# Kernel tuning notes

Hardware: AMD Instinct MI355X
Metric: run time of the kernel (lower is better)

The kernel has to match this reference:

```python
import jax, jax.numpy as jnp
import numpy as np

B, IN_CH, OUT_CH, T, N_STATE, FACTOR = 8, 128, 128, 16384, 256, 2
DT = 1.0
LN_EPS = 1e-5


def setup_inputs() -> dict:
    key = jax.random.key(0)
    k = jax.random.split(key, 5)
    x = jax.random.normal(k[0], (B, IN_CH, T), jnp.float32)
    raw_lambda = jnp.zeros((N_STATE,), jnp.float32)
    B_c = jax.random.normal(k[1], (IN_CH, N_STATE), jnp.float32) * (1.0 / np.sqrt(IN_CH))
    C_mat = jax.random.normal(k[2], (N_STATE, OUT_CH), jnp.float32) * (1.0 / np.sqrt(N_STATE))
    ln_gamma = jnp.ones((OUT_CH,), jnp.float32)
    ln_beta = jnp.zeros((OUT_CH,), jnp.float32)
    # Conv1d(out_ch*factor, out_ch, kernel_size=1): weight (out, in), bias (out,)
    W = jax.random.normal(k[3], (OUT_CH, OUT_CH * FACTOR), jnp.float32) * (1.0 / np.sqrt(OUT_CH * FACTOR))
    b = jax.random.normal(k[4], (OUT_CH,), jnp.float32) * 0.01
    return {"x": x, "raw_lambda": raw_lambda, "B_c": B_c, "C_mat": C_mat,
            "ln_gamma": ln_gamma, "ln_beta": ln_beta, "W": W, "b": b}


def reference(x, raw_lambda, B_c, C_mat, ln_gamma, ln_beta, W, b):
    # --- SSMLayerZOH ---
    lam = -jax.nn.softplus(raw_lambda)              # (N,) continuous diag, < 0
    A_d = jnp.exp(lam * DT)                         # ZOH discretized diag
    B_d = B_c * ((A_d - 1.0) / lam)[None, :]        # (IN, N)
    v = jnp.einsum('bct,cn->tbn', x, B_d)           # per-step input injection

    def step(s, vt):
        s = s * A_d + vt
        return s, s

    s0 = jnp.zeros((x.shape[0], lam.shape[0]), x.dtype)
    _, ss = jax.lax.scan(step, s0, v)               # (T, B, N)
    y = jnp.einsum('tbn,no->bto', ss, C_mat)        # (B, T, OUT)

    # --- LayerNorm(out_ch) + SiLU ---
    mu = jnp.mean(y, axis=-1, keepdims=True)
    var = jnp.mean((y - mu) ** 2, axis=-1, keepdims=True)
    h = (y - mu) / jnp.sqrt(var + LN_EPS) * ln_gamma + ln_beta
    h = h * jax.nn.sigmoid(h)                       # SiLU

    # --- Resample (factor > 1 branch): downsample T, stack factor into channels ---
    h = jnp.transpose(h, (0, 2, 1))                 # (B, OUT, T)
    Bn, C, Tt = h.shape
    hr = h.reshape(Bn, C, Tt // FACTOR, FACTOR)
    hr = jnp.transpose(hr, (0, 1, 3, 2)).reshape(Bn, C * FACTOR, Tt // FACTOR)
    out = jnp.einsum('bct,oc->bot', hr, W) + b[None, :, None]  # conv1x1
    return out
```

## Files before the change

kernel.cpp:

```cpp
#include <hip/hip_runtime.h>

#define BATCH 8
#define CIN 128
#define OCH 128
#define T_LEN 16384
#define NS 256
#define CHUNK 64
#define NCHUNK (T_LEN / CHUNK)
#define THALF (T_LEN / 2)
#define SCHUNK 8192
#define HROW 132
#define NCHK 8

typedef __attribute__((ext_vector_type(8))) short bf16x8;
typedef __attribute__((ext_vector_type(4))) float f32x4;
typedef __attribute__((ext_vector_type(4))) unsigned int u32x4;

__device__ __forceinline__ unsigned int pk2(float lo, float hi) {
  unsigned int d;
  asm("v_cvt_pk_bf16_f32 %0, %1, %2" : "=v"(d) : "v"(lo), "v"(hi));
  return d;
}
__device__ __forceinline__ unsigned short f2bf(float f) {
  unsigned int u = __float_as_uint(f);
  u += 0x7fffu + ((u >> 16) & 1u);
  return (unsigned short)(u >> 16);
}
__device__ __forceinline__ float softplusf_(float v) {
  return (v > 20.0f) ? v : log1pf(expf(v));
}
__device__ __forceinline__ void rawbar() {
  __builtin_amdgcn_sched_barrier(0);
  asm volatile("s_waitcnt lgkmcnt(0)" ::: "memory");
  __builtin_amdgcn_sched_barrier(0);
  __builtin_amdgcn_s_barrier();
  __builtin_amdgcn_sched_barrier(0);
}

__global__ __launch_bounds__(256) void k_prep(
    const float* __restrict__ rl, const float* __restrict__ Bc,
    const float* __restrict__ Cm, const float* __restrict__ W,
    unsigned short* __restrict__ BdT, unsigned short* __restrict__ CT,
    unsigned short* __restrict__ Wb, float* __restrict__ Ad, float* __restrict__ rL,
    float* __restrict__ PWf)
{
  const int tid = blockIdx.x * 256 + threadIdx.x;
  if (tid < NS * CIN) {
    const int n = tid >> 7, c = tid & 127;
    float lam = -softplusf_(rl[n]);
    float ad = expf(lam);
    float sc = (ad - 1.0f) / lam;
    BdT[tid] = f2bf(Bc[c * NS + n] * sc);
  } else if (tid < 2 * NS * CIN) {
    const int i = tid - NS * CIN;
    const int o = i >> 8, n = i & 255;
    CT[i] = f2bf(Cm[n * OCH + o]);
  } else if (tid < 3 * NS * CIN) {
    const int i = tid - 2 * NS * CIN;
    Wb[i] = f2bf(W[i]);
  } else if (tid < 3 * NS * CIN + NS) {
    const int n = tid - 3 * NS * CIN;
    float lam = -softplusf_(rl[n]);
    Ad[n] = expf(lam);
    rL[n] = expf(lam * (float)CHUNK);
  } else if (tid < 3 * NS * CIN + NS + 32 * NS) {
    const int i = tid - (3 * NS * CIN + NS);
    const int tp = i >> 8, n = i & 255;
    float lam = -softplusf_(rl[n]);
    PWf[i] = expf(lam * (float)(2 * tp + 1));
  }
}

__global__ __launch_bounds__(256) void k_combine(float* __restrict__ carry,
                                                 const float* __restrict__ rL)
{
  const int b = blockIdx.x >> 5;
  const int ng = blockIdx.x & 31;
  const int t = threadIdx.x;
  __shared__ float Y[8][NCHUNK];
  float* base = carry + ((size_t)b * NCHUNK + t) * NS + ng * 8;
  #pragma unroll
  for (int i4 = 0; i4 < 2; ++i4) {
    float4 q = *(const float4*)(base + i4 * 4);
    Y[i4 * 4 + 0][t] = q.x; Y[i4 * 4 + 1][t] = q.y;
    Y[i4 * 4 + 2][t] = q.z; Y[i4 * 4 + 3][t] = q.w;
  }
  float rp[8];
  #pragma unroll
  for (int i = 0; i < 8; ++i) rp[i] = rL[ng * 8 + i];
  __syncthreads();
  for (int d = 1; d < NCHUNK; d <<= 1) {
    float tmp[8];
    #pragma unroll
    for (int i = 0; i < 8; ++i) tmp[i] = (t >= d) ? Y[i][t - d] : 0.0f;
    __syncthreads();
    #pragma unroll
    for (int i = 0; i < 8; ++i) { Y[i][t] += rp[i] * tmp[i]; rp[i] *= rp[i]; }
    __syncthreads();
  }
  const int tm = (t == 0) ? 0 : (t - 1);
  #pragma unroll
  for (int i4 = 0; i4 < 2; ++i4) {
    float a = Y[i4 * 4 + 0][tm], bb = Y[i4 * 4 + 1][tm];
    float c = Y[i4 * 4 + 2][tm], dd = Y[i4 * 4 + 3][tm];
    float4 q;
    q.x = (t == 0) ? 0.0f : a;  q.y = (t == 0) ? 0.0f : bb;
    q.z = (t == 0) ? 0.0f : c;  q.w = (t == 0) ? 0.0f : dd;
    *(float4*)(base + i4 * 4) = q;
  }
}

__global__ __launch_bounds__(512, 4) void k_scan(
    const float* __restrict__ x,
    const unsigned short* __restrict__ BdT,
    const float* __restrict__ Ad,
    unsigned int* __restrict__ s0,
    float* __restrict__ carry)
{
  const int bid = blockIdx.x;
  const int b = bid >> 8;
  const int kc = bid & 255;
  const int tid = threadIdx.x;
  const int w = tid >> 6, l = tid & 63, l15 = l & 15, g = l >> 4;

  __shared__ __align__(16) unsigned int Xt[64 * 64];

  {
    const int c2 = w * 8 + (l & 7);
    const int t0b = (l >> 3) * 8;
    const float* r0 = x + ((size_t)(b * CIN + 2 * c2)) * T_LEN + kc * CHUNK + t0b;
    const f32x4 xa0 = *(const f32x4*)r0;
    const f32x4 xa1 = *(const f32x4*)(r0 + 4);
    const f32x4 xb0 = *(const f32x4*)(r0 + T_LEN);
    const f32x4 xb1 = *(const f32x4*)(r0 + T_LEN + 4);
    #pragma unroll
    for (int k = 0; k < 8; ++k) {
      const int t = t0b + k;
      const float va = (k < 4) ? xa0[k & 3] : xa1[k & 3];
      const float vb = (k < 4) ? xb0[k & 3] : xb1[k & 3];
      Xt[t * 64 + (c2 ^ ((t & 7) << 2))] = pk2(va, vb);
    }
  }

  bf16x8 Bf[2][4];
  #pragma unroll
  for (int nt = 0; nt < 2; ++nt)
    #pragma unroll
    for (int kt = 0; kt < 4; ++kt)
      Bf[nt][kt] = *(const bf16x8*)&BdT[(w * 32 + nt * 16 + l15) * CIN + kt * 32 + g * 8];

  float A1[2], A2[2], A3[2], A4[2], A8[2], A16[2], A4G[2], M1[2], M2[2];
  #pragma unroll
  for (int nt = 0; nt < 2; ++nt) {
    const float a1 = Ad[w * 32 + nt * 16 + l15];
    A1[nt] = a1; A2[nt] = a1 * a1; A3[nt] = A2[nt] * a1; A4[nt] = A2[nt] * A2[nt];
    A8[nt] = A4[nt] * A4[nt]; A16[nt] = A8[nt] * A8[nt];
    float a4g = 1.0f;
    if (g & 1) a4g *= A4[nt];
    if (g & 2) a4g *= A8[nt];
    A4G[nt] = a4g;
    M1[nt] = (g >= 1) ? A4[nt] : 0.0f;
    M2[nt] = (g >= 2) ? A8[nt] : 0.0f;
  }
  __syncthreads();

  f32x4 vac[4][2] = {};
  #pragma unroll
  for (int kt = 0; kt < 4; ++kt) {
    bf16x8 afr[4];
    #pragma unroll
    for (int mt = 0; mt < 4; ++mt)
      afr[mt] = *(const bf16x8*)&Xt[(mt * 16 + l15) * 64 + ((kt * 16 + g * 4) ^ ((l15 & 7) << 2))];
    #pragma unroll
    for (int nt = 0; nt < 2; ++nt)
      #pragma unroll
      for (int mt = 0; mt < 4; ++mt)
        vac[mt][nt] = __builtin_amdgcn_mfma_f32_16x16x32_bf16(afr[mt], Bf[nt][kt], vac[mt][nt], 0, 0, 0);
  }

  float crv[2];
  #pragma unroll
  for (int nt = 0; nt < 2; ++nt) {
    float cr = 0.0f;
    #pragma unroll
    for (int mt = 0; mt < 4; ++mt) {
      const float p0 = vac[mt][nt][0];
      const float p1 = fmaf(A1[nt], p0, vac[mt][nt][1]);
      const float p2 = fmaf(A1[nt], p1, vac[mt][nt][2]);
      const float p3 = fmaf(A1[nt], p2, vac[mt][nt][3]);
      float c0 = p3;
      float u = __shfl_up(c0, 16);
      c0 = fmaf(M1[nt], u, c0);
      u = __shfl_up(c0, 32);
      c0 = fmaf(M2[nt], u, c0);
      float e = __shfl_up(c0, 16);
      e = (g == 0) ? 0.0f : e;
      const float seed = fmaf(A4G[nt], cr, e);
      vac[mt][nt][0] = fmaf(A1[nt], seed, p0);
      vac[mt][nt][1] = fmaf(A2[nt], seed, p1);
      vac[mt][nt][2] = fmaf(A3[nt], seed, p2);
      vac[mt][nt][3] = fmaf(A4[nt], seed, p3);
      const float ctop = __shfl(c0, 48 + l15);
      cr = fmaf(A16[nt], cr, ctop);
    }
    crv[nt] = cr;
  }

  unsigned int* sc = s0 + (size_t)(b * NCHUNK + kc) * SCHUNK;
  #pragma unroll
  for (int mt = 0; mt < 4; ++mt)
    #pragma unroll
    for (int nt = 0; nt < 2; ++nt) {
      const int n = w * 32 + nt * 16 + l15;
      #pragma unroll
      for (int rp = 0; rp < 2; ++rp) {
        const int tp = mt * 8 + g * 2 + rp;
        sc[tp * 256 + n] = pk2(vac[mt][nt][rp * 2], vac[mt][nt][rp * 2 + 1]);
      }
    }
  if (g == 0) {
    #pragma unroll
    for (int nt = 0; nt < 2; ++nt)
      carry[((size_t)b * NCHUNK + kc) * NS + (w * 32 + nt * 16 + l15)] = crv[nt];
  }
}

__global__ __launch_bounds__(512, 2) void k_apply(
    const unsigned int* __restrict__ S,
    const unsigned short* __restrict__ CT,
    const unsigned short* __restrict__ Wb,
    const float* __restrict__ PWf,
    const float* __restrict__ Ad,
    const float* __restrict__ carry,
    const float* __restrict__ lng, const float* __restrict__ lnb,
    const float* __restrict__ bias,
    float* __restrict__ out)
{
  const int bid = blockIdx.x;
  const int b = bid / (NCHUNK / NCHK);
  const int kc0 = (bid % (NCHUNK / NCHK)) * NCHK;
  const int tid = threadIdx.x;
  const int w = tid >> 6, l = tid & 63, l15 = l & 15, g = l >> 4;
  const int tt = w >> 2, oq = w & 3;

  __shared__ __align__(16) unsigned short V2a[64 * 256];
  __shared__ __align__(16) unsigned short V2b[64 * 256];
  __shared__ __align__(16) unsigned int Hra[32 * HROW];
  __shared__ __align__(16) unsigned int Hrb[32 * HROW];
  __shared__ __align__(16) float Lexf[2][64 * 8];

  const f32x4 adv = *(const f32x4*)&Ad[4 * l];

  bf16x8 ctf[8][2];
  #pragma unroll
  for (int kt = 0; kt < 8; ++kt)
    #pragma unroll
    for (int ot = 0; ot < 2; ++ot)
      ctf[kt][ot] = *(const bf16x8*)&CT[(oq * 32 + ot * 16 + l15) * NS + kt * 32 + g * 8];
  bf16x8 wf[8];
  #pragma unroll
  for (int kt = 0; kt < 8; ++kt)
    wf[kt] = *(const bf16x8*)&Wb[(w * 16 + l15) * NS + kt * 32 + g * 8];
  f32x4 pwv[4];
  #pragma unroll
  for (int r = 0; r < 4; ++r)
    pwv[r] = *(const f32x4*)&PWf[(r * 8 + w) * 256 + 4 * l];
  const float ga0 = lng[oq * 32 + l15],      be0 = lnb[oq * 32 + l15];
  const float ga1 = lng[oq * 32 + 16 + l15], be1 = lnb[oq * 32 + 16 + l15];
  const float bia = bias[w * 16 + l15];

  u32x4 sa0, sa1, sa2, sa3, sb0, sb1, sb2, sb3;
  f32x4 sda, sdb;

#define LOAD_ST(KC, T0, T1, T2, T3, SD) do {                                \
    const unsigned int* scb_ = S + (size_t)(b * NCHUNK + (KC)) * SCHUNK;    \
    T0 = *(const u32x4*)&scb_[0 * 2048 + tid * 4];                          \
    T1 = *(const u32x4*)&scb_[1 * 2048 + tid * 4];                          \
    T2 = *(const u32x4*)&scb_[2 * 2048 + tid * 4];                          \
    T3 = *(const u32x4*)&scb_[3 * 2048 + tid * 4];                          \
    SD = *(const f32x4*)&carry[((size_t)b * NCHUNK + (KC)) * NS + 4 * l];   \
  } while (0)

#define CORRECT_ROW(DSTV, QV, RR, SD) do {                                  \
    const float e00 = SD[0] * pwv[RR][0];                                   \
    const float e01 = SD[1] * pwv[RR][1];                                   \
    const float e02 = SD[2] * pwv[RR][2];                                   \
    const float e03 = SD[3] * pwv[RR][3];                                   \
    const float lo0 = __uint_as_float(QV[0] << 16) + e00;                   \
    const float hi0 = __uint_as_float(QV[0] & 0xffff0000u) + e00 * adv[0];  \
    const float lo1 = __uint_as_float(QV[1] << 16) + e01;                   \
    const float hi1 = __uint_as_float(QV[1] & 0xffff0000u) + e01 * adv[1];  \
    const float lo2 = __uint_as_float(QV[2] << 16) + e02;                   \
    const float hi2 = __uint_as_float(QV[2] & 0xffff0000u) + e02 * adv[2];  \
    const float lo3 = __uint_as_float(QV[3] << 16) + e03;                   \
    const float hi3 = __uint_as_float(QV[3] & 0xffff0000u) + e03 * adv[3];  \
    const int t0_ = ((RR) * 8 + w) * 2;                                     \
    const int t1_ = t0_ + 1;                                                \
    uint2 wlo; wlo.x = pk2(lo0, lo1); wlo.y = pk2(lo2, lo3);                \
    uint2 whi; whi.x = pk2(hi0, hi1); whi.y = pk2(hi2, hi3);                \
    *(uint2*)&DSTV[t0_ * 256 + ((((l >> 1) ^ ((t0_ & 7) << 2)) << 3) | ((l & 1) << 2))] = wlo; \
    *(uint2*)&DSTV[t1_ * 256 + ((((l >> 1) ^ ((t1_ & 7) << 2)) << 3) | ((l & 1) << 2))] = whi; \
  } while (0)

#define CORRECT_STORE(DSTV, T0, T1, T2, T3, SD) do {                        \
    CORRECT_ROW(DSTV, T0, 0, SD);                                           \
    CORRECT_ROW(DSTV, T1, 1, SD);                                           \
    CORRECT_ROW(DSTV, T2, 2, SD);                                           \
    CORRECT_ROW(DSTV, T3, 3, SD);                                           \
  } while (0)

#define YGEMM(V2X, YAC, IDX) do {                                           \
    _Pragma("unroll")                                                       \
    for (int kt = 0; kt < 8; ++kt) {                                        \
      bf16x8 As0, As1;                                                      \
      {                                                                     \
        const int t0 = tt * 32 + l15;                                       \
        As0 = *(const bf16x8*)&V2X[t0 * 256 + (((kt * 4 + g) ^ ((t0 & 7) << 2)) << 3)]; \
        const int t1 = tt * 32 + 16 + l15;                                  \
        As1 = *(const bf16x8*)&V2X[t1 * 256 + (((kt * 4 + g) ^ ((t1 & 7) << 2)) << 3)]; \
      }                                                                     \
      _Pragma("unroll")                                                     \
      for (int ot = 0; ot < 2; ++ot) {                                      \
        YAC[0][ot] = __builtin_amdgcn_mfma_f32_16x16x32_bf16(As0, ctf[kt][ot], YAC[0][ot], 0, 0, 0); \
        YAC[1][ot] = __builtin_amdgcn_mfma_f32_16x16x32_bf16(As1, ctf[kt][ot], YAC[1][ot], 0, 0, 0); \
      }                                                                     \
    }                                                                       \
    _Pragma("unroll")                                                       \
    for (int mt = 0; mt < 2; ++mt)                                          \
      _Pragma("unroll")                                                     \
      for (int r = 0; r < 4; ++r) {                                         \
        float s1 = YAC[mt][0][r] + YAC[mt][1][r];                           \
        float s2 = YAC[mt][0][r] * YAC[mt][0][r] + YAC[mt][1][r] * YAC[mt][1][r]; \
        _Pragma("unroll")                                                   \
        for (int d = 1; d < 16; d <<= 1) { s1 += __shfl_xor(s1, d); s2 += __shfl_xor(s2, d); } \
        if (l15 == 0) {                                                     \
          const int t = tt * 32 + mt * 16 + g * 4 + r;                      \
          *(float2*)&Lexf[IDX][t * 8 + oq * 2] = make_float2(s1, s2);       \
        }                                                                   \
      }                                                                     \
  } while (0)

#define LNSILU(HRX, YAC, IDX) do {                                          \
    _Pragma("unroll")                                                       \
    for (int mt = 0; mt < 2; ++mt) {                                        \
      float mu[4], rs[4];                                                   \
      _Pragma("unroll")                                                     \
      for (int r = 0; r < 4; ++r) {                                         \
        const int t = tt * 32 + mt * 16 + g * 4 + r;                        \
        const float4 f0 = *(const float4*)&Lexf[IDX][t * 8];                \
        const float4 f1 = *(const float4*)&Lexf[IDX][t * 8 + 4];            \
        const float m = (f0.x + f0.z + f1.x + f1.z) * (1.0f / 128.0f);      \
        const float va = (f0.y + f0.w + f1.y + f1.w) * (1.0f / 128.0f) - m * m; \
        mu[r] = m;                                                          \
        rs[r] = rsqrtf(va + 1e-5f);                                         \
      }                                                                     \
      _Pragma("unroll")                                                     \
      for (int ot = 0; ot < 2; ++ot) {                                      \
        const int o = oq * 32 + ot * 16 + l15;                              \
        const float ga = ot ? ga1 : ga0;                                    \
        const float be = ot ? be1 : be0;                                    \
        _Pragma("unroll")                                                   \
        for (int rp = 0; rp < 2; ++rp) {                                    \
          float h0 = (YAC[mt][ot][rp * 2] - mu[rp * 2]) * rs[rp * 2] * ga + be; \
          h0 = h0 * __builtin_amdgcn_rcpf(1.0f + __expf(-h0));              \
          float h1 = (YAC[mt][ot][rp * 2 + 1] - mu[rp * 2 + 1]) * rs[rp * 2 + 1] * ga + be; \
          h1 = h1 * __builtin_amdgcn_rcpf(1.0f + __expf(-h1));              \
          const int t2 = tt * 16 + mt * 8 + g * 2 + rp;                     \
          HRX[t2 * HROW + o] = pk2(h0, h1);                                 \
        }                                                                   \
      }                                                                     \
    }                                                                       \
  } while (0)

#define OUTGEMM(HRX, KC) do {                                               \
    f32x4 oac0 = {}, oac1 = {};                                             \
    _Pragma("unroll")                                                       \
    for (int kt = 0; kt < 8; ++kt) {                                        \
      bf16x8 Aa0, Aa1;                                                      \
      {                                                                     \
        union { bf16x8 v; u32x4 u; } Ax;                                    \
        Ax.u = *(const u32x4*)&HRX[(l15) * HROW + kt * 16 + g * 4];         \
        Aa0 = Ax.v;                                                         \
        Ax.u = *(const u32x4*)&HRX[(16 + l15) * HROW + kt * 16 + g * 4];    \
        Aa1 = Ax.v;                                                         \
      }                                                                     \
      oac0 = __builtin_amdgcn_mfma_f32_16x16x32_bf16(Aa0, wf[kt], oac0, 0, 0, 0); \
      oac1 = __builtin_amdgcn_mfma_f32_16x16x32_bf16(Aa1, wf[kt], oac1, 0, 0, 0); \
    }                                                                       \
    const int o = w * 16 + l15;                                             \
    float4 q0;                                                              \
    q0.x = oac0[0] + bia; q0.y = oac0[1] + bia;                             \
    q0.z = oac0[2] + bia; q0.w = oac0[3] + bia;                             \
    *(float4*)(out + ((size_t)(b * OCH + o)) * THALF + (KC) * 32 + g * 4) = q0; \
    float4 q1;                                                              \
    q1.x = oac1[0] + bia; q1.y = oac1[1] + bia;                             \
    q1.z = oac1[2] + bia; q1.w = oac1[3] + bia;                             \
    *(float4*)(out + ((size_t)(b * OCH + o)) * THALF + (KC) * 32 + 16 + g * 4) = q1; \
  } while (0)

  LOAD_ST(kc0 + 0, sa0, sa1, sa2, sa3, sda);
  CORRECT_STORE(V2a, sa0, sa1, sa2, sa3, sda);
  LOAD_ST(kc0 + 1, sb0, sb1, sb2, sb3, sdb);
  CORRECT_STORE(V2b, sb0, sb1, sb2, sb3, sdb);
  LOAD_ST(kc0 + 2, sa0, sa1, sa2, sa3, sda);
  LOAD_ST(kc0 + 3, sb0, sb1, sb2, sb3, sdb);
  rawbar();

  #pragma unroll 1
  for (int i = 0; i < NCHK / 2; ++i) {
    const int kcA = kc0 + 2 * i;
    const int kcB = kcA + 1;

    f32x4 yacA[2][2] = {};
    f32x4 yacB[2][2] = {};
    YGEMM(V2a, yacA, 0);
    YGEMM(V2b, yacB, 1);
    rawbar();

    LNSILU(Hra, yacA, 0);
    LNSILU(Hrb, yacB, 1);
    if (i + 1 < NCHK / 2) {
      CORRECT_STORE(V2a, sa0, sa1, sa2, sa3, sda);
      CORRECT_STORE(V2b, sb0, sb1, sb2, sb3, sdb);
      if (i + 2 < NCHK / 2) {
        LOAD_ST(kcA + 4, sa0, sa1, sa2, sa3, sda);
        LOAD_ST(kcB + 4, sb0, sb1, sb2, sb3, sdb);
      }
    }
    rawbar();

    OUTGEMM(Hra, kcA);
    OUTGEMM(Hrb, kcB);
  }
#undef LOAD_ST
#undef CORRECT_ROW
#undef CORRECT_STORE
#undef YGEMM
#undef LNSILU
#undef OUTGEMM
}

extern "C" void kernel_launch(void* const* d_in, const int* in_sizes, int n_in,
                              void* d_out, int out_size, void* d_ws, size_t ws_size,
                              hipStream_t stream) {
  const float* x    = (const float*)d_in[0];
  const float* rl   = (const float*)d_in[1];
  const float* Bc   = (const float*)d_in[2];
  const float* Cm   = (const float*)d_in[3];
  const float* lng  = (const float*)d_in[4];
  const float* lnb  = (const float*)d_in[5];
  const float* W    = (const float*)d_in[6];
  const float* bias = (const float*)d_in[7];
  float* out = (float*)d_out;

  char* ws = (char*)d_ws;
  unsigned short* BdT = (unsigned short*)(ws);
  unsigned short* CT  = (unsigned short*)(ws + 65536);
  unsigned short* Wb  = (unsigned short*)(ws + 131072);
  float* Ad    = (float*)(ws + 196608);
  float* rL    = (float*)(ws + 197632);
  float* PWf   = (float*)(ws + 198656);
  float* carry = (float*)(ws + 231424);
  unsigned int* S = (unsigned int*)(ws + 231424 + 2097152);

  k_prep<<<417, 256, 0, stream>>>(rl, Bc, Cm, W, BdT, CT, Wb, Ad, rL, PWf);
  k_scan<<<BATCH * NCHUNK, 512, 0, stream>>>(x, BdT, Ad, S, carry);
  k_combine<<<BATCH * 32, 256, 0, stream>>>(carry, rL);
  k_apply<<<BATCH * (NCHUNK / NCHK), 512, 0, stream>>>(S, CT, Wb, PWf, Ad, carry,
                                                       lng, lnb, bias, out);
}
```

Measured before the change: 93.95 us.

## Process four chunks per scan block with double-buffered LDS and register prefetch

k_scan now loops over four consecutive time chunks per block instead of one. It keeps the B_d fragments and A powers in registers across chunks and prefetches the next chunk's x into registers while computing the current one, using a double-buffered LDS tile. The grid shrinks fourfold and launch bounds drop to 3 waves per SIMD. This amortizes setup loads and overlaps global loads with MFMA work, at the cost of fewer blocks and possibly lower occupancy.

```diff
diff --git a/kernel.cpp b/kernel.cpp
--- a/kernel.cpp
+++ b/kernel.cpp
@@ -11,6 +11,7 @@
 #define SCHUNK 8192
 #define HROW 132
 #define NCHK 8
+#define SCHK 4
 
 typedef __attribute__((ext_vector_type(8))) short bf16x8;
 typedef __attribute__((ext_vector_type(4))) float f32x4;
@@ -110,7 +111,7 @@
   }
 }
 
-__global__ __launch_bounds__(512, 4) void k_scan(
+__global__ __launch_bounds__(512, 3) void k_scan(
     const float* __restrict__ x,
     const unsigned short* __restrict__ BdT,
     const float* __restrict__ Ad,
@@ -118,29 +119,12 @@
     float* __restrict__ carry)
 {
   const int bid = blockIdx.x;
-  const int b = bid >> 8;
-  const int kc = bid & 255;
+  const int b = bid / (NCHUNK / SCHK);
+  const int kc0 = (bid % (NCHUNK / SCHK)) * SCHK;
   const int tid = threadIdx.x;
   const int w = tid >> 6, l = tid & 63, l15 = l & 15, g = l >> 4;
 
-  __shared__ __align__(16) unsigned int Xt[64 * 64];
-
-  {
-    const int c2 = w * 8 + (l & 7);
-    const int t0b = (l >> 3) * 8;
-    const float* r0 = x + ((size_t)(b * CIN + 2 * c2)) * T_LEN + kc * CHUNK + t0b;
-    const f32x4 xa0 = *(const f32x4*)r0;
-    const f32x4 xa1 = *(const f32x4*)(r0 + 4);
-    const f32x4 xb0 = *(const f32x4*)(r0 + T_LEN);
-    const f32x4 xb1 = *(const f32x4*)(r0 + T_LEN + 4);
-    #pragma unroll
-    for (int k = 0; k < 8; ++k) {
-      const int t = t0b + k;
-      const float va = (k < 4) ? xa0[k & 3] : xa1[k & 3];
-      const float vb = (k < 4) ? xb0[k & 3] : xb1[k & 3];
-      Xt[t * 64 + (c2 ^ ((t & 7) << 2))] = pk2(va, vb);
-    }
-  }
+  __shared__ __align__(16) unsigned int Xt[2][64 * 64];
 
   bf16x8 Bf[2][4];
   #pragma unroll
@@ -162,66 +146,102 @@
     M1[nt] = (g >= 1) ? A4[nt] : 0.0f;
     M2[nt] = (g >= 2) ? A8[nt] : 0.0f;
   }
-  __syncthreads();
-
-  f32x4 vac[4][2] = {};
-  #pragma unroll
-  for (int kt = 0; kt < 4; ++kt) {
-    bf16x8 afr[4];
-    #pragma unroll
-    for (int mt = 0; mt < 4; ++mt)
-      afr[mt] = *(const bf16x8*)&Xt[(mt * 16 + l15) * 64 + ((kt * 16 + g * 4) ^ ((l15 & 7) << 2))];
-    #pragma unroll
-    for (int nt = 0; nt < 2; ++nt)
+
+  const int c2 = w * 8 + (l & 7);
+  const int t0b = (l >> 3) * 8;
+  const float* xbase = x + ((size_t)(b * CIN + 2 * c2)) * T_LEN + t0b;
+
+  f32x4 xa0, xa1, xb0, xb1;
+  {
+    const float* r0 = xbase + kc0 * CHUNK;
+    xa0 = *(const f32x4*)r0;
+    xa1 = *(const f32x4*)(r0 + 4);
+    xb0 = *(const f32x4*)(r0 + T_LEN);
+    xb1 = *(const f32x4*)(r0 + T_LEN + 4);
+  }
+
+  int cur = 0;
+  #pragma unroll 1
+  for (int i = 0; i < SCHK; ++i) {
+    const int kc = kc0 + i;
+
+    #pragma unroll
+    for (int k = 0; k < 8; ++k) {
+      const int t = t0b + k;
+      const float va = (k < 4) ? xa0[k & 3] : xa1[k & 3];
+      const float vb = (k < 4) ? xb0[k & 3] : xb1[k & 3];
+      Xt[cur][t * 64 + (c2 ^ ((t & 7) << 2))] = pk2(va, vb);
+    }
+    rawbar();
+
+    if (i + 1 < SCHK) {
+      const float* r0 = xbase + (kc + 1) * CHUNK;
+      xa0 = *(const f32x4*)r0;
+      xa1 = *(const f32x4*)(r0 + 4);
+      xb0 = *(const f32x4*)(r0 + T_LEN);
+      xb1 = *(const f32x4*)(r0 + T_LEN + 4);
+    }
+
+    f32x4 vac[4][2] = {};
+    #pragma unroll
+    for (int kt = 0; kt < 4; ++kt) {
+      bf16x8 afr[4];
       #pragma unroll
       for (int mt = 0; mt < 4; ++mt)
-        vac[mt][nt] = __builtin_amdgcn_mfma_f32_16x16x32_bf16(afr[mt], Bf[nt][kt], vac[mt][nt], 0, 0, 0);
-  }
-
-  float crv[2];
-  #pragma unroll
-  for (int nt = 0; nt < 2; ++nt) {
-    float cr = 0.0f;
-    #pragma unroll
-    for (int mt = 0; mt < 4; ++mt) {
-      const float p0 = vac[mt][nt][0];
-      const float p1 = fmaf(A1[nt], p0, vac[mt][nt][1]);
-      const float p2 = fmaf(A1[nt], p1, vac[mt][nt][2]);
-      const float p3 = fmaf(A1[nt], p2, vac[mt][nt][3]);
-      float c0 = p3;
-      float u = __shfl_up(c0, 16);
-      c0 = fmaf(M1[nt], u, c0);
-      u = __shfl_up(c0, 32);
-      c0 = fmaf(M2[nt], u, c0);
-      float e = __shfl_up(c0, 16);
-      e = (g == 0) ? 0.0f : e;
-      const float seed = fmaf(A4G[nt], cr, e);
-      vac[mt][nt][0] = fmaf(A1[nt], seed, p0);
-      vac[mt][nt][1] = fmaf(A2[nt], seed, p1);
-      vac[mt][nt][2] = fmaf(A3[nt], seed, p2);
-      vac[mt][nt][3] = fmaf(A4[nt], seed, p3);
-      const float ctop = __shfl(c0, 48 + l15);
-      cr = fmaf(A16[nt], cr, ctop);
-    }
-    crv[nt] = cr;
-  }
-
-  unsigned int* sc = s0 + (size_t)(b * NCHUNK + kc) * SCHUNK;
-  #pragma unroll
-  for (int mt = 0; mt < 4; ++mt)
+        afr[mt] = *(const bf16x8*)&Xt[cur][(mt * 16 + l15) * 64 + ((kt * 16 + g * 4) ^ ((l15 & 7) << 2))];
+      #pragma unroll
+      for (int nt = 0; nt < 2; ++nt)
+        #pragma unroll
+        for (int mt = 0; mt < 4; ++mt)
+          vac[mt][nt] = __builtin_amdgcn_mfma_f32_16x16x32_bf16(afr[mt], Bf[nt][kt], vac[mt][nt], 0, 0, 0);
+    }
+
+    float crv[2];
     #pragma unroll
     for (int nt = 0; nt < 2; ++nt) {
-      const int n = w * 32 + nt * 16 + l15;
+      float cr = 0.0f;
       #pragma unroll
-      for (int rp = 0; rp < 2; ++rp) {
-        const int tp = mt * 8 + g * 2 + rp;
-        sc[tp * 256 + n] = pk2(vac[mt][nt][rp * 2], vac[mt][nt][rp * 2 + 1]);
+      for (int mt = 0; mt < 4; ++mt) {
+        const float p0 = vac[mt][nt][0];
+        const float p1 = fmaf(A1[nt], p0, vac[mt][nt][1]);
+        const float p2 = fmaf(A1[nt], p1, vac[mt][nt][2]);
+        const float p3 = fmaf(A1[nt], p2, vac[mt][nt][3]);
+        float c0 = p3;
+        float u = __shfl_up(c0, 16);
+        c0 = fmaf(M1[nt], u, c0);
+        u = __shfl_up(c0, 32);
+        c0 = fmaf(M2[nt], u, c0);
+        float e = __shfl_up(c0, 16);
+        e = (g == 0) ? 0.0f : e;
+        const float seed = fmaf(A4G[nt], cr, e);
+        vac[mt][nt][0] = fmaf(A1[nt], seed, p0);
+        vac[mt][nt][1] = fmaf(A2[nt], seed, p1);
+        vac[mt][nt][2] = fmaf(A3[nt], seed, p2);
+        vac[mt][nt][3] = fmaf(A4[nt], seed, p3);
+        const float ctop = __shfl(c0, 48 + l15);
+        cr = fmaf(A16[nt], cr, ctop);
       }
-    }
-  if (g == 0) {
-    #pragma unroll
-    for (int nt = 0; nt < 2; ++nt)
-      carry[((size_t)b * NCHUNK + kc) * NS + (w * 32 + nt * 16 + l15)] = crv[nt];
+      crv[nt] = cr;
+    }
+
+    unsigned int* sc = s0 + (size_t)(b * NCHUNK + kc) * SCHUNK;
+    #pragma unroll
+    for (int mt = 0; mt < 4; ++mt)
+      #pragma unroll
+      for (int nt = 0; nt < 2; ++nt) {
+        const int n = w * 32 + nt * 16 + l15;
+        #pragma unroll
+        for (int rp = 0; rp < 2; ++rp) {
+          const int tp = mt * 8 + g * 2 + rp;
+          sc[tp * 256 + n] = pk2(vac[mt][nt][rp * 2], vac[mt][nt][rp * 2 + 1]);
+        }
+      }
+    if (g == 0) {
+      #pragma unroll
+      for (int nt = 0; nt < 2; ++nt)
+        carry[((size_t)b * NCHUNK + kc) * NS + (w * 32 + nt * 16 + l15)] = crv[nt];
+    }
+    cur ^= 1;
   }
 }
 
@@ -464,7 +484,7 @@
   unsigned int* S = (unsigned int*)(ws + 231424 + 2097152);
 
   k_prep<<<417, 256, 0, stream>>>(rl, Bc, Cm, W, BdT, CT, Wb, Ad, rL, PWf);
-  k_scan<<<BATCH * NCHUNK, 512, 0, stream>>>(x, BdT, Ad, S, carry);
+  k_scan<<<BATCH * (NCHUNK / SCHK), 512, 0, stream>>>(x, BdT, Ad, S, carry);
   k_combine<<<BATCH * 32, 256, 0, stream>>>(carry, rL);
   k_apply<<<BATCH * (NCHUNK / NCHK), 512, 0, stream>>>(S, CT, Wb, PWf, Ad, carry,
                                                        lng, lnb, bias, out);
```

Result: faster. 91.94 us (-2.1%).
